# Performance work log

Measured on AMD Instinct MI355X. Metric: run time of the kernel, lower is better.

The kernel has to match this reference:

```python
import jax, jax.numpy as jnp
import numpy as np

N_NODES = 100_000
N_EDGES = 1_600_000
IN_DIM = 64
OUT_DIM = 64
EPS = 1e-5


def setup_inputs() -> dict:
    key = jax.random.key(0)
    k1, k2, k3, k4, k5, k6 = jax.random.split(key, 6)
    node = jax.random.normal(k1, (N_NODES, 3), dtype=jnp.float32)
    features = jax.random.normal(k2, (N_NODES, IN_DIM), dtype=jnp.float32)
    # src column covers every node so torch.unique(edges[:,0]) == arange(N_NODES)
    src = (jnp.arange(N_EDGES, dtype=jnp.int64) % N_NODES)
    dst = jax.random.randint(k3, (N_EDGES,), 0, N_NODES, dtype=jnp.int64)
    edges = jnp.stack([src, dst], axis=1)
    # torch.nn.Linear weight: [out_dim, in_dim+3], no bias
    W = jax.random.normal(k4, (OUT_DIM, IN_DIM + 3), dtype=jnp.float32) / np.sqrt(IN_DIM + 3)
    gamma = jnp.ones((OUT_DIM,), dtype=jnp.float32)
    beta = jnp.zeros((OUT_DIM,), dtype=jnp.float32)
    return {"node": node, "features": features, "W": W, "gamma": gamma,
            "beta": beta, "edges": edges}


def reference(node, features, W, gamma, beta, edges):
    src = edges[:, 0]
    dst = edges[:, 1]
    # gather + concat: [E, in_dim + 3]
    msg = jnp.concatenate([features[dst], node[dst] - node[src]], axis=1)
    # linear (no bias): [E, out_dim]
    h = msg @ W.T
    # BatchNorm1d (training mode: biased batch statistics over E rows)
    mean = jnp.mean(h, axis=0)
    var = jnp.mean(jnp.square(h - mean), axis=0)
    h = (h - mean) * jax.lax.rsqrt(var + EPS) * gamma + beta
    h = jax.nn.relu(h)
    # scatter_reduce amax with include_self=True on a zeros tensor:
    # per-destination max, including the initial 0 (relu output >= 0 anyway)
    n = node.shape[0]
    pooled = jnp.zeros((n, h.shape[1]), dtype=features.dtype).at[src].max(h)
    return pooled
```

## Files before the change

kernel.cpp:

```cpp
#include <hip/hip_runtime.h>

#define N_NODES 100000
#define N_EDGES 1600000
#define EPS 1e-5f
#define NG 12500

typedef __bf16    bf16x8 __attribute__((ext_vector_type(8)));
typedef _Float16  f16x2  __attribute__((ext_vector_type(2)));
typedef _Float16  f16x4  __attribute__((ext_vector_type(4)));
typedef float     f32x4  __attribute__((ext_vector_type(4)));
typedef unsigned int u32;
typedef u32       u32x4  __attribute__((ext_vector_type(4)));

__device__ __forceinline__ u32 pkmax(u32 a, u32 b) {
  u32 d; asm("v_pk_max_f16 %0,%1,%2" : "=v"(d) : "v"(a), "v"(b)); return d;
}
__device__ __forceinline__ u32 pkmin(u32 a, u32 b) {
  u32 d; asm("v_pk_min_f16 %0,%1,%2" : "=v"(d) : "v"(a), "v"(b)); return d;
}
__device__ __forceinline__ float halves_sum(u32 v, float c) {
  f16x2 p = __builtin_bit_cast(f16x2, v);
#if __has_builtin(__builtin_amdgcn_fdot2)
  f16x2 one2 = {(_Float16)1.0f, (_Float16)1.0f};
  return __builtin_amdgcn_fdot2(p, one2, c, false);
#else
  return c + (float)p[0] + (float)p[1];
#endif
}
__device__ __forceinline__ float halves_sq(u32 v, float c) {
  f16x2 p = __builtin_bit_cast(f16x2, v);
#if __has_builtin(__builtin_amdgcn_fdot2)
  return __builtin_amdgcn_fdot2(p, p, c, false);
#else
  float a = (float)p[0], b = (float)p[1];
  return fmaf(a, a, fmaf(b, b, c));
#endif
}

__global__ __launch_bounds__(256) void gemm_kernel(
    const float* __restrict__ nodep, const float* __restrict__ feat,
    const float* __restrict__ W, unsigned short* __restrict__ g,
    float* __restrict__ accum) {
  if (blockIdx.x == 0) {
    for (int k = threadIdx.x; k < 1024; k += 256) accum[k] = 0.f;
  }

  const int lane = threadIdx.x & 63;
  const int wave = (int)((blockIdx.x * blockDim.x + threadIdx.x) >> 6);
  const int c    = lane & 15;
  const int quad = lane >> 4;
  if (wave >= N_NODES / 16) return;

  bf16x8 Bfrag[4][3];
#pragma unroll
  for (int t = 0; t < 4; ++t) {
    const float* wrow = W + (t * 16 + c) * 67;
#pragma unroll
    for (int s = 0; s < 3; ++s) {
#pragma unroll
      for (int j = 0; j < 8; ++j) {
        int k = s * 32 + quad * 8 + j;
        Bfrag[t][s][j] = (k < 67) ? (__bf16)wrow[k] : (__bf16)0.0f;
      }
    }
  }

  const int v = wave * 16 + c;
  const f32x4* f4 = (const f32x4*)(feat + (size_t)v * 64 + quad * 8);
  f32x4 fa = f4[0], fb = f4[1];
  const f32x4* f4b = (const f32x4*)(feat + (size_t)v * 64 + 32 + quad * 8);
  f32x4 fc = f4b[0], fd = f4b[1];
  bf16x8 A0, A1;
#pragma unroll
  for (int j = 0; j < 4; ++j) {
    A0[j] = (__bf16)fa[j]; A0[j + 4] = (__bf16)fb[j];
    A1[j] = (__bf16)fc[j]; A1[j + 4] = (__bf16)fd[j];
  }
  bf16x8 A2;
#pragma unroll
  for (int j = 0; j < 8; ++j) A2[j] = (__bf16)0.0f;
  if (quad == 0) {
    const float* np = nodep + (size_t)v * 3;
    A2[0] = (__bf16)np[0];
    A2[1] = (__bf16)np[1];
    A2[2] = (__bf16)np[2];
  }

#pragma unroll
  for (int t = 0; t < 4; ++t) {
    f32x4 acc = {0.f, 0.f, 0.f, 0.f};
    acc = __builtin_amdgcn_mfma_f32_16x16x32_bf16(A0, Bfrag[t][0], acc, 0, 0, 0);
    acc = __builtin_amdgcn_mfma_f32_16x16x32_bf16(A1, Bfrag[t][1], acc, 0, 0, 0);
    acc = __builtin_amdgcn_mfma_f32_16x16x32_bf16(A2, Bfrag[t][2], acc, 0, 0, 0);
    unsigned short* gp = g + (size_t)(wave * 16 + quad * 4) * 64 + t * 16 + c;
#pragma unroll
    for (int r = 0; r < 4; ++r)
      gp[r * 64] = __builtin_bit_cast(unsigned short, (_Float16)acc[r]);
  }
}

__global__ __launch_bounds__(256) void gather_kernel(
    const float* __restrict__ nodep, const int* __restrict__ edges,
    const _Float16* __restrict__ g, const float* __restrict__ W,
    _Float16* __restrict__ gmax, _Float16* __restrict__ gmin,
    float* __restrict__ accum) {
  const int lane = threadIdx.x & 63;
  const int wave = (int)((blockIdx.x * blockDim.x + threadIdx.x) >> 6);
  const int ch = lane & 7;
  const int s  = lane >> 3;
  const int i  = wave * 8 + s;

  int idx[16];
  const int* ep = edges + 2 * i + 1;
#pragma unroll
  for (int k = 0; k < 16; ++k) idx[k] = ep[2 * k * N_NODES];

  u32x4 r[16];
#pragma unroll
  for (int k = 0; k < 16; ++k)
    r[k] = *(const u32x4*)(g + (size_t)idx[k] * 64 + ch * 8);

  const float* np = nodep + (size_t)i * 3;
  const float nx = np[0], ny = np[1], nz = np[2];

  float Sn[8], sq[8];
#pragma unroll
  for (int j = 0; j < 8; ++j) { Sn[j] = 0.f; sq[j] = 0.f; }
  u32 mx[4], mn[4];
#pragma unroll
  for (int p = 0; p < 8; ++p) {
    const u32x4 va = r[2 * p], vb = r[2 * p + 1];
#pragma unroll
    for (int q = 0; q < 4; ++q) {
      u32 m  = pkmax(va[q], vb[q]);
      u32 n2 = pkmin(va[q], vb[q]);
      if (p == 0) { mx[q] = m; mn[q] = n2; }
      else        { mx[q] = pkmax(mx[q], m); mn[q] = pkmin(mn[q], n2); }
      u32 plo = __builtin_amdgcn_perm(va[q], vb[q], 0x01000504u);
      u32 phi = __builtin_amdgcn_perm(va[q], vb[q], 0x03020706u);
      Sn[2 * q]     = halves_sum(plo, Sn[2 * q]);
      Sn[2 * q + 1] = halves_sum(phi, Sn[2 * q + 1]);
      sq[2 * q]     = halves_sq(plo, sq[2 * q]);
      sq[2 * q + 1] = halves_sq(phi, sq[2 * q + 1]);
    }
  }
  u32x4 wm = {mx[0], mx[1], mx[2], mx[3]};
  *(u32x4*)(gmax + (size_t)i * 64 + ch * 8) = wm;
  u32x4 wn = {mn[0], mn[1], mn[2], mn[3]};
  *(u32x4*)(gmin + (size_t)i * 64 + ch * 8) = wn;

  float px[8], py[8], pz[8];
#pragma unroll
  for (int j = 0; j < 8; ++j) {
    px[j] = nx * Sn[j]; py[j] = ny * Sn[j]; pz[j] = nz * Sn[j];
  }
  float Lx = nx, Ly = ny, Lz = nz;
  float Mxx = nx * nx, Myy = ny * ny, Mzz = nz * nz;
  float Mxy = nx * ny, Mxz = nx * nz, Myz = ny * nz;
#pragma unroll
  for (int step = 8; step < 64; step <<= 1) {
#pragma unroll
    for (int j = 0; j < 8; ++j) {
      Sn[j] += __shfl_xor(Sn[j], step, 64);
      sq[j] += __shfl_xor(sq[j], step, 64);
      px[j] += __shfl_xor(px[j], step, 64);
      py[j] += __shfl_xor(py[j], step, 64);
      pz[j] += __shfl_xor(pz[j], step, 64);
    }
    Lx  += __shfl_xor(Lx, step, 64);  Ly  += __shfl_xor(Ly, step, 64);
    Lz  += __shfl_xor(Lz, step, 64);
    Mxx += __shfl_xor(Mxx, step, 64); Myy += __shfl_xor(Myy, step, 64);
    Mzz += __shfl_xor(Mzz, step, 64); Mxy += __shfl_xor(Mxy, step, 64);
    Mxz += __shfl_xor(Mxz, step, 64); Myz += __shfl_xor(Myz, step, 64);
  }

  __shared__ float sred[4][128];
  const int w = (int)(threadIdx.x >> 6);
  if (lane < 8) {
#pragma unroll
    for (int j = 0; j < 8; ++j) {
      int col = ch * 8 + j;
      const float* wr = W + col * 67 + 64;
      float w0 = wr[0], w1 = wr[1], w2 = wr[2];
      float sumc = w0 * Lx + w1 * Ly + w2 * Lz;
      float cS   = w0 * px[j] + w1 * py[j] + w2 * pz[j];
      float wMw  = w0 * w0 * Mxx + w1 * w1 * Myy + w2 * w2 * Mzz
                 + 2.f * (w0 * w1 * Mxy + w0 * w2 * Mxz + w1 * w2 * Myz);
      sred[w][col]      = Sn[j] - 16.f * sumc;
      sred[w][64 + col] = sq[j] - 2.f * cS + 16.f * wMw;
    }
  }
  __syncthreads();
  const int t = threadIdx.x;
  if (t < 128) {
    float v = (sred[0][t] + sred[1][t]) + (sred[2][t] + sred[3][t]);
    atomicAdd(accum + 128 * (blockIdx.x & 7) + t, v);
  }
}

__global__ __launch_bounds__(256) void finalize_kernel(
    const _Float16* __restrict__ gmax, const _Float16* __restrict__ gmin,
    const float* __restrict__ accum, const float* __restrict__ gamma,
    const float* __restrict__ beta, const float* __restrict__ nodep,
    const float* __restrict__ W, float* __restrict__ out) {
  __shared__ __align__(16) float ssl[128];
  __shared__ float wnl[192];
  const int t = threadIdx.x;
  if (t < 64) {
    float a = 0.f, b = 0.f;
#pragma unroll
    for (int rp = 0; rp < 8; ++rp) {
      a += accum[rp * 128 + t];
      b += accum[rp * 128 + 64 + t];
    }
    const float inv_ne = 1.0f / (float)N_EDGES;
    float mean = a * inv_ne;
    float var  = fmaxf(b * inv_ne - mean * mean, 0.f);
    float sc   = gamma[t] * rsqrtf(var + EPS);
    ssl[t]      = sc;
    ssl[64 + t] = beta[t] - mean * sc;
    wnl[3 * t]     = W[t * 67 + 64];
    wnl[3 * t + 1] = W[t * 67 + 65];
    wnl[3 * t + 2] = W[t * 67 + 66];
  }
  __syncthreads();

  const int idx = (blockIdx.x * 256 + t) * 4;
  const int i = idx >> 6, d0 = idx & 63;
  const float nx = nodep[3 * i], ny = nodep[3 * i + 1], nz = nodep[3 * i + 2];
  f32x4 scv = *(const f32x4*)&ssl[d0];
  bool needmax = (scv[0] >= 0.f) | (scv[1] >= 0.f) | (scv[2] >= 0.f) | (scv[3] >= 0.f);
  bool needmin = (scv[0] < 0.f) | (scv[1] < 0.f) | (scv[2] < 0.f) | (scv[3] < 0.f);
  f16x4 gx = {}, gn = {};
  if (needmax) gx = *(const f16x4*)(gmax + idx);
  if (needmin) gn = *(const f16x4*)(gmin + idx);
  f32x4 o;
#pragma unroll
  for (int j = 0; j < 4; ++j) {
    int d = d0 + j;
    float sc = scv[j], shf = ssl[64 + d];
    float v = (sc >= 0.f) ? (float)gx[j] : (float)gn[j];
    float c = fmaf(wnl[3 * d + 2], nz, fmaf(wnl[3 * d + 1], ny, wnl[3 * d] * nx));
    o[j] = fmaxf(fmaf(v - c, sc, shf), 0.f);
  }
  *(f32x4*)(out + idx) = o;
}

extern "C" void kernel_launch(void* const* d_in, const int* in_sizes, int n_in,
                              void* d_out, int out_size, void* d_ws, size_t ws_size,
                              hipStream_t stream) {
  const float* nodep = (const float*)d_in[0];
  const float* feat  = (const float*)d_in[1];
  const float* W     = (const float*)d_in[2];
  const float* gamma = (const float*)d_in[3];
  const float* beta  = (const float*)d_in[4];
  const int*   edges = (const int*)d_in[5];

  char* ws = (char*)d_ws;
  unsigned short* g = (unsigned short*)ws;
  _Float16* gmax = (_Float16*)(ws + 12800000);
  _Float16* gmin = (_Float16*)(ws + 25600000);
  float* accum   = (float*)(ws + 38400000);
  float* out     = (float*)d_out;

  gemm_kernel<<<1563, 256, 0, stream>>>(nodep, feat, W, g, accum);
  gather_kernel<<<NG / 4, 256, 0, stream>>>(nodep, edges, (const _Float16*)g,
                                            W, gmax, gmin, accum);
  finalize_kernel<<<6250, 256, 0, stream>>>(gmax, gmin, accum, gamma, beta,
                                            nodep, W, out);
}
```

Before: 146.7 us.

## Split g into 8-column chunks so gather blocks cover one chunk

Stores the per-node projection g (and gmax/gmin) as eight column-chunk planes of 8 halves each instead of row-major 64 wide. Each gather block now handles one column chunk for 256 nodes, one node per thread, so the random gathers in a block hit a 1.6 MB plane that fits in cache better. The block also computes the per-edge position correction directly per thread, which removes the shuffle reductions of the moment terms. In exchange it launches eight times as many blocks, reads edge indices and node positions eight times over, and uses 16-byte per-lane gathers with less coalescing per wave.

```diff
diff --git a/kernel.cpp b/kernel.cpp
--- a/kernel.cpp
+++ b/kernel.cpp
@@ -3,11 +3,11 @@
 #define N_NODES 100000
 #define N_EDGES 1600000
 #define EPS 1e-5f
-#define NG 12500
+#define CHUNK_STRIDE (N_NODES * 8)
 
 typedef __bf16    bf16x8 __attribute__((ext_vector_type(8)));
 typedef _Float16  f16x2  __attribute__((ext_vector_type(2)));
-typedef _Float16  f16x4  __attribute__((ext_vector_type(4)));
+typedef _Float16  f16x8  __attribute__((ext_vector_type(8)));
 typedef float     f32x4  __attribute__((ext_vector_type(4)));
 typedef unsigned int u32;
 typedef u32       u32x4  __attribute__((ext_vector_type(4)));
@@ -44,7 +44,6 @@
   if (blockIdx.x == 0) {
     for (int k = threadIdx.x; k < 1024; k += 256) accum[k] = 0.f;
   }
-
   const int lane = threadIdx.x & 63;
   const int wave = (int)((blockIdx.x * blockDim.x + threadIdx.x) >> 6);
   const int c    = lane & 15;
@@ -56,11 +55,11 @@
   for (int t = 0; t < 4; ++t) {
     const float* wrow = W + (t * 16 + c) * 67;
 #pragma unroll
-    for (int s = 0; s < 3; ++s) {
+    for (int s2 = 0; s2 < 3; ++s2) {
 #pragma unroll
       for (int j = 0; j < 8; ++j) {
-        int k = s * 32 + quad * 8 + j;
-        Bfrag[t][s][j] = (k < 67) ? (__bf16)wrow[k] : (__bf16)0.0f;
+        int k = s2 * 32 + quad * 8 + j;
+        Bfrag[t][s2][j] = (k < 67) ? (__bf16)wrow[k] : (__bf16)0.0f;
       }
     }
   }
@@ -92,109 +91,106 @@
     acc = __builtin_amdgcn_mfma_f32_16x16x32_bf16(A0, Bfrag[t][0], acc, 0, 0, 0);
     acc = __builtin_amdgcn_mfma_f32_16x16x32_bf16(A1, Bfrag[t][1], acc, 0, 0, 0);
     acc = __builtin_amdgcn_mfma_f32_16x16x32_bf16(A2, Bfrag[t][2], acc, 0, 0, 0);
-    unsigned short* gp = g + (size_t)(wave * 16 + quad * 4) * 64 + t * 16 + c;
+    const int d = t * 16 + c;
+    unsigned short* gp = g + (size_t)(d >> 3) * CHUNK_STRIDE
+                           + (size_t)(wave * 16 + quad * 4) * 8 + (d & 7);
 #pragma unroll
     for (int r = 0; r < 4; ++r)
-      gp[r * 64] = __builtin_bit_cast(unsigned short, (_Float16)acc[r]);
+      gp[r * 8] = __builtin_bit_cast(unsigned short, (_Float16)acc[r]);
   }
 }
 
 __global__ __launch_bounds__(256) void gather_kernel(
     const float* __restrict__ nodep, const int* __restrict__ edges,
-    const _Float16* __restrict__ g, const float* __restrict__ W,
+    const unsigned short* __restrict__ g, const float* __restrict__ W,
     _Float16* __restrict__ gmax, _Float16* __restrict__ gmin,
     float* __restrict__ accum) {
-  const int lane = threadIdx.x & 63;
-  const int wave = (int)((blockIdx.x * blockDim.x + threadIdx.x) >> 6);
-  const int ch = lane & 7;
-  const int s  = lane >> 3;
-  const int i  = wave * 8 + s;
-
-  int idx[16];
-  const int* ep = edges + 2 * i + 1;
-#pragma unroll
-  for (int k = 0; k < 16; ++k) idx[k] = ep[2 * k * N_NODES];
-
-  u32x4 r[16];
-#pragma unroll
-  for (int k = 0; k < 16; ++k)
-    r[k] = *(const u32x4*)(g + (size_t)idx[k] * 64 + ch * 8);
-
-  const float* np = nodep + (size_t)i * 3;
-  const float nx = np[0], ny = np[1], nz = np[2];
-
-  float Sn[8], sq[8];
-#pragma unroll
-  for (int j = 0; j < 8; ++j) { Sn[j] = 0.f; sq[j] = 0.f; }
-  u32 mx[4], mn[4];
-#pragma unroll
-  for (int p = 0; p < 8; ++p) {
-    const u32x4 va = r[2 * p], vb = r[2 * p + 1];
-#pragma unroll
-    for (int q = 0; q < 4; ++q) {
-      u32 m  = pkmax(va[q], vb[q]);
-      u32 n2 = pkmin(va[q], vb[q]);
-      if (p == 0) { mx[q] = m; mn[q] = n2; }
-      else        { mx[q] = pkmax(mx[q], m); mn[q] = pkmin(mn[q], n2); }
-      u32 plo = __builtin_amdgcn_perm(va[q], vb[q], 0x01000504u);
-      u32 phi = __builtin_amdgcn_perm(va[q], vb[q], 0x03020706u);
-      Sn[2 * q]     = halves_sum(plo, Sn[2 * q]);
-      Sn[2 * q + 1] = halves_sum(phi, Sn[2 * q + 1]);
-      sq[2 * q]     = halves_sq(plo, sq[2 * q]);
-      sq[2 * q + 1] = halves_sq(phi, sq[2 * q + 1]);
-    }
-  }
-  u32x4 wm = {mx[0], mx[1], mx[2], mx[3]};
-  *(u32x4*)(gmax + (size_t)i * 64 + ch * 8) = wm;
-  u32x4 wn = {mn[0], mn[1], mn[2], mn[3]};
-  *(u32x4*)(gmin + (size_t)i * 64 + ch * 8) = wn;
-
-  float px[8], py[8], pz[8];
-#pragma unroll
-  for (int j = 0; j < 8; ++j) {
-    px[j] = nx * Sn[j]; py[j] = ny * Sn[j]; pz[j] = nz * Sn[j];
-  }
-  float Lx = nx, Ly = ny, Lz = nz;
-  float Mxx = nx * nx, Myy = ny * ny, Mzz = nz * nz;
-  float Mxy = nx * ny, Mxz = nx * nz, Myz = ny * nz;
-#pragma unroll
-  for (int step = 8; step < 64; step <<= 1) {
+  const int tid  = (int)threadIdx.x;
+  const int lane = tid & 63;
+  const int cb   = (int)(blockIdx.x & 7);
+  const int i    = (int)(blockIdx.x >> 3) * 256 + tid;
+
+  __shared__ float wnl[24];
+  __shared__ float sred[4][16];
+  if (tid < 8) {
+    const int col = cb * 8 + tid;
+    wnl[3 * tid]     = W[col * 67 + 64];
+    wnl[3 * tid + 1] = W[col * 67 + 65];
+    wnl[3 * tid + 2] = W[col * 67 + 66];
+  }
+  __syncthreads();
+
+  float sh[8], sq[8];
+#pragma unroll
+  for (int j = 0; j < 8; ++j) { sh[j] = 0.f; sq[j] = 0.f; }
+
+  if (i < N_NODES) {
+    int idx[16];
+    const int* ep = edges + 2 * i + 1;
+#pragma unroll
+    for (int k = 0; k < 16; ++k) idx[k] = ep[2 * k * N_NODES];
+    const unsigned short* gt = g + (size_t)cb * CHUNK_STRIDE;
+    u32x4 r[16];
+#pragma unroll
+    for (int k = 0; k < 16; ++k)
+      r[k] = *(const u32x4*)(gt + (size_t)idx[k] * 8);
+
+    const float* np = nodep + (size_t)i * 3;
+    const float nx = np[0], ny = np[1], nz = np[2];
+
+    float Sn[8], sqg[8];
+#pragma unroll
+    for (int j = 0; j < 8; ++j) { Sn[j] = 0.f; sqg[j] = 0.f; }
+    u32 mx[4], mn[4];
+#pragma unroll
+    for (int p = 0; p < 8; ++p) {
+      const u32x4 va = r[2 * p], vb = r[2 * p + 1];
+#pragma unroll
+      for (int q = 0; q < 4; ++q) {
+        u32 m  = pkmax(va[q], vb[q]);
+        u32 n2 = pkmin(va[q], vb[q]);
+        if (p == 0) { mx[q] = m; mn[q] = n2; }
+        else        { mx[q] = pkmax(mx[q], m); mn[q] = pkmin(mn[q], n2); }
+        u32 plo = __builtin_amdgcn_perm(va[q], vb[q], 0x01000504u);
+        u32 phi = __builtin_amdgcn_perm(va[q], vb[q], 0x03020706u);
+        Sn[2 * q]      = halves_sum(plo, Sn[2 * q]);
+        Sn[2 * q + 1]  = halves_sum(phi, Sn[2 * q + 1]);
+        sqg[2 * q]     = halves_sq(plo, sqg[2 * q]);
+        sqg[2 * q + 1] = halves_sq(phi, sqg[2 * q + 1]);
+      }
+    }
+    u32x4 wm = {mx[0], mx[1], mx[2], mx[3]};
+    *(u32x4*)(gmax + (size_t)cb * CHUNK_STRIDE + (size_t)i * 8) = wm;
+    u32x4 wn4 = {mn[0], mn[1], mn[2], mn[3]};
+    *(u32x4*)(gmin + (size_t)cb * CHUNK_STRIDE + (size_t)i * 8) = wn4;
 #pragma unroll
     for (int j = 0; j < 8; ++j) {
-      Sn[j] += __shfl_xor(Sn[j], step, 64);
+      const float* wp = wnl + 3 * j;
+      float cj = fmaf(wp[2], nz, fmaf(wp[1], ny, wp[0] * nx));
+      sh[j] = Sn[j] - 16.f * cj;
+      sq[j] = sqg[j] + cj * fmaf(16.f, cj, -2.f * Sn[j]);
+    }
+  }
+
+#pragma unroll
+  for (int step = 1; step < 64; step <<= 1) {
+#pragma unroll
+    for (int j = 0; j < 8; ++j) {
+      sh[j] += __shfl_xor(sh[j], step, 64);
       sq[j] += __shfl_xor(sq[j], step, 64);
-      px[j] += __shfl_xor(px[j], step, 64);
-      py[j] += __shfl_xor(py[j], step, 64);
-      pz[j] += __shfl_xor(pz[j], step, 64);
-    }
-    Lx  += __shfl_xor(Lx, step, 64);  Ly  += __shfl_xor(Ly, step, 64);
-    Lz  += __shfl_xor(Lz, step, 64);
-    Mxx += __shfl_xor(Mxx, step, 64); Myy += __shfl_xor(Myy, step, 64);
-    Mzz += __shfl_xor(Mzz, step, 64); Mxy += __shfl_xor(Mxy, step, 64);
-    Mxz += __shfl_xor(Mxz, step, 64); Myz += __shfl_xor(Myz, step, 64);
-  }
-
-  __shared__ float sred[4][128];
-  const int w = (int)(threadIdx.x >> 6);
-  if (lane < 8) {
-#pragma unroll
-    for (int j = 0; j < 8; ++j) {
-      int col = ch * 8 + j;
-      const float* wr = W + col * 67 + 64;
-      float w0 = wr[0], w1 = wr[1], w2 = wr[2];
-      float sumc = w0 * Lx + w1 * Ly + w2 * Lz;
-      float cS   = w0 * px[j] + w1 * py[j] + w2 * pz[j];
-      float wMw  = w0 * w0 * Mxx + w1 * w1 * Myy + w2 * w2 * Mzz
-                 + 2.f * (w0 * w1 * Mxy + w0 * w2 * Mxz + w1 * w2 * Myz);
-      sred[w][col]      = Sn[j] - 16.f * sumc;
-      sred[w][64 + col] = sq[j] - 2.f * cS + 16.f * wMw;
-    }
+    }
+  }
+  const int w = tid >> 6;
+  if (lane == 0) {
+#pragma unroll
+    for (int j = 0; j < 8; ++j) { sred[w][j] = sh[j]; sred[w][8 + j] = sq[j]; }
   }
   __syncthreads();
-  const int t = threadIdx.x;
-  if (t < 128) {
-    float v = (sred[0][t] + sred[1][t]) + (sred[2][t] + sred[3][t]);
-    atomicAdd(accum + 128 * (blockIdx.x & 7) + t, v);
+  if (tid < 16) {
+    float v = (sred[0][tid] + sred[1][tid]) + (sred[2][tid] + sred[3][tid]);
+    const int col = cb * 8 + (tid & 7);
+    const int off = (tid < 8) ? col : (64 + col);
+    atomicAdd(accum + 128 * ((int)(blockIdx.x >> 3) & 7) + off, v);
   }
 }
 
@@ -225,25 +221,34 @@
   }
   __syncthreads();
 
-  const int idx = (blockIdx.x * 256 + t) * 4;
-  const int i = idx >> 6, d0 = idx & 63;
+  const int q  = (int)(blockIdx.x * 256) + t;
+  const int i  = q >> 3, cb = q & 7, d0 = cb * 8;
   const float nx = nodep[3 * i], ny = nodep[3 * i + 1], nz = nodep[3 * i + 2];
-  f32x4 scv = *(const f32x4*)&ssl[d0];
-  bool needmax = (scv[0] >= 0.f) | (scv[1] >= 0.f) | (scv[2] >= 0.f) | (scv[3] >= 0.f);
-  bool needmin = (scv[0] < 0.f) | (scv[1] < 0.f) | (scv[2] < 0.f) | (scv[3] < 0.f);
-  f16x4 gx = {}, gn = {};
-  if (needmax) gx = *(const f16x4*)(gmax + idx);
-  if (needmin) gn = *(const f16x4*)(gmin + idx);
-  f32x4 o;
-#pragma unroll
-  for (int j = 0; j < 4; ++j) {
-    int d = d0 + j;
-    float sc = scv[j], shf = ssl[64 + d];
+  f32x4 sc0 = *(const f32x4*)&ssl[d0];
+  f32x4 sc1 = *(const f32x4*)&ssl[d0 + 4];
+  bool needmax = (sc0[0] >= 0.f) | (sc0[1] >= 0.f) | (sc0[2] >= 0.f) |
+                 (sc0[3] >= 0.f) | (sc1[0] >= 0.f) | (sc1[1] >= 0.f) |
+                 (sc1[2] >= 0.f) | (sc1[3] >= 0.f);
+  bool needmin = (sc0[0] < 0.f) | (sc0[1] < 0.f) | (sc0[2] < 0.f) |
+                 (sc0[3] < 0.f) | (sc1[0] < 0.f) | (sc1[1] < 0.f) |
+                 (sc1[2] < 0.f) | (sc1[3] < 0.f);
+  f16x8 gx = {}, gn = {};
+  if (needmax) gx = *(const f16x8*)(gmax + (size_t)cb * CHUNK_STRIDE + (size_t)i * 8);
+  if (needmin) gn = *(const f16x8*)(gmin + (size_t)cb * CHUNK_STRIDE + (size_t)i * 8);
+  f32x4 o0, o1;
+#pragma unroll
+  for (int j = 0; j < 8; ++j) {
+    const int d = d0 + j;
+    float sc = (j < 4) ? sc0[j] : sc1[j - 4];
+    float shf = ssl[64 + d];
     float v = (sc >= 0.f) ? (float)gx[j] : (float)gn[j];
     float c = fmaf(wnl[3 * d + 2], nz, fmaf(wnl[3 * d + 1], ny, wnl[3 * d] * nx));
-    o[j] = fmaxf(fmaf(v - c, sc, shf), 0.f);
-  }
-  *(f32x4*)(out + idx) = o;
+    float r = fmaxf(fmaf(v - c, sc, shf), 0.f);
+    if (j < 4) o0[j] = r; else o1[j - 4] = r;
+  }
+  float* op = out + (size_t)i * 64 + d0;
+  *(f32x4*)op       = o0;
+  *(f32x4*)(op + 4) = o1;
 }
 
 extern "C" void kernel_launch(void* const* d_in, const int* in_sizes, int n_in,
@@ -264,8 +269,8 @@
   float* out     = (float*)d_out;
 
   gemm_kernel<<<1563, 256, 0, stream>>>(nodep, feat, W, g, accum);
-  gather_kernel<<<NG / 4, 256, 0, stream>>>(nodep, edges, (const _Float16*)g,
-                                            W, gmax, gmin, accum);
-  finalize_kernel<<<6250, 256, 0, stream>>>(gmax, gmin, accum, gamma, beta,
-                                            nodep, W, out);
-}
+  gather_kernel<<<8 * ((N_NODES + 255) / 256), 256, 0, stream>>>(
+      nodep, edges, g, W, gmax, gmin, accum);
+  finalize_kernel<<<(N_NODES * 8) / 256, 256, 0, stream>>>(
+      gmax, gmin, accum, gamma, beta, nodep, W, out);
+}
```

Measured after the change: 175.0 us. 1.19x slower.
